# Optimization experiments

Hardware: AMD Instinct MI355X
Metric: run time of the kernel (lower is better)

Reference implementation:

```python
import jax, jax.numpy as jnp
import numpy as np


def setup_inputs() -> dict:
    key = jax.random.key(0)
    ks = jax.random.split(key, 5)
    b, t, e, h = 8, 1024, 256, 8
    w = lambda k, shape: jax.random.normal(k, shape, dtype=jnp.float32) * 0.02
    return {
        "x": jax.random.normal(ks[0], (b, t, e), dtype=jnp.float32),
        "Wq": w(ks[1], (e, e * h)), "bq": jnp.zeros((e * h,), jnp.float32),
        "Wk": w(ks[2], (e, e * h)), "bk": jnp.zeros((e * h,), jnp.float32),
        "Wv": w(ks[3], (e, e * h)), "bv": jnp.zeros((e * h,), jnp.float32),
        "Wu": w(ks[4], (e * h, e)), "bu": jnp.zeros((e,), jnp.float32),
    }


def reference(x, Wq, bq, Wk, bk, Wv, bv, Wu, bu):
    b, t, e = x.shape
    h = Wq.shape[1] // e  # each head has FULL width e in this module
    q = (x @ Wq + bq).reshape(b, t, h, e)
    k = (x @ Wk + bk).reshape(b, t, h, e)
    v = (x @ Wv + bv).reshape(b, t, h, e)
    # scores: (b, h, t, t), scaled by sqrt(e) as in the original
    scores = jnp.einsum('bihe,bjhe->bhij', q, k) / jnp.sqrt(jnp.asarray(e, jnp.float32))
    i = jnp.arange(t)[:, None]
    j = jnp.arange(t)[None, :]
    # mask mode 'first': triu(offset=0) -> -inf, i.e. query i sees only j < i
    scores = jnp.where(j >= i, -jnp.inf, scores)
    # row 0 is fully masked (torch softmax -> NaN, then zeroed post-softmax);
    # make it finite first so softmax is well-defined, then zero the attention row
    scores = jnp.where(i == 0, 0.0, scores)
    att = jax.nn.softmax(scores, axis=-1)
    att = jnp.where(i == 0, 0.0, att)
    out = jnp.einsum('bhij,bjhe->bihe', att, v).reshape(b, t, h * e)
    return out @ Wu + bu
```

## Files before the change

### kernel.cpp

```cpp
#include <hip/hip_runtime.h>

typedef unsigned short u16;
typedef short bf16x8 __attribute__((ext_vector_type(8)));
typedef float f32x4 __attribute__((ext_vector_type(4)));

static __device__ __forceinline__ u16 f2bf(float f) {
  union { float f; unsigned u; } a; a.f = f;
  unsigned r = a.u + 0x7fffu + ((a.u >> 16) & 1u);
  return (u16)(r >> 16);
}

static __device__ __forceinline__ bf16x8 as_bf(int4 v) {
  union { int4 i; bf16x8 b; } u; u.i = v; return u.b;
}

#define GLDS16(g, l)                                         \
  __builtin_amdgcn_global_load_lds(                          \
      (const __attribute__((address_space(1))) void*)(g),    \
      (__attribute__((address_space(3))) void*)(l), 16, 0, 0)

__global__ __launch_bounds__(256) void cvt_f32_bf16(const float* __restrict__ in,
                                                    u16* __restrict__ out, int n8) {
  int i = blockIdx.x * 256 + threadIdx.x;
  if (i >= n8) return;
  const float4* p = (const float4*)in + (size_t)i * 2;
  float4 a = p[0], b = p[1];
  union { u16 s[8]; int4 v; } u2;
  u2.s[0] = f2bf(a.x); u2.s[1] = f2bf(a.y); u2.s[2] = f2bf(a.z); u2.s[3] = f2bf(a.w);
  u2.s[4] = f2bf(b.x); u2.s[5] = f2bf(b.y); u2.s[6] = f2bf(b.z); u2.s[7] = f2bf(b.w);
  ((int4*)out)[i] = u2.v;
}

__global__ __launch_bounds__(256) void transpose_w(const float* __restrict__ in,
                                                   u16* __restrict__ out, int R, int C) {
  int T = blockIdx.x * 256 + threadIdx.x;
  int c = T % C;
  int rg = T / C;
  int r0 = rg * 32;
  __align__(16) u16 tmp[32];
#pragma unroll
  for (int j = 0; j < 32; ++j) tmp[j] = f2bf(in[(size_t)(r0 + j) * C + c]);
#pragma unroll
  for (int q = 0; q < 4; ++q)
    *(int4*)(out + (size_t)c * R + r0 + q * 8) = *(int4*)&tmp[q * 8];
}

__global__ __launch_bounds__(256) void transpose_v(const u16* __restrict__ V,
                                                   u16* __restrict__ Vt) {
  int T = blockIdx.x * 256 + threadIdx.x;
  int e = T & 255, tg = (T >> 8) & 31, bh = T >> 13;
  int b = bh >> 3, h = bh & 7;
  const u16* src = V + (size_t)(b * 1024 + tg * 32) * 2048 + h * 256 + e;
  __align__(16) u16 tmp[32];
#pragma unroll
  for (int j = 0; j < 32; ++j) tmp[j] = src[(size_t)j * 2048];
  u16* dst = Vt + (size_t)(bh * 256 + e) * 1024 + tg * 32;
#pragma unroll
  for (int q = 0; q < 4; ++q) *(int4*)(dst + q * 8) = *(int4*)&tmp[q * 8];
}

template <int BM, int BN, bool OUTBF>
__global__ __launch_bounds__(256) void gemm_bt(const u16* __restrict__ A,
                                               const u16* __restrict__ Bt,
                                               const float* __restrict__ bias0,
                                               const float* __restrict__ bias1,
                                               const float* __restrict__ bias2,
                                               void* __restrict__ Cout,
                                               int M, int N, int K) {
  constexpr int BK = 64;
  constexpr int TM = BM / 2 / 16, TN = BN / 2 / 16;
  constexpr int nA = BM / 32, nB = BN / 32;
  __shared__ int4 As4[BM * 8];
  __shared__ int4 Bs4[BN * 8];
  const int tid = threadIdx.x;
  const int w = tid >> 6, lane = tid & 63, lq = lane & 15, quad = lane >> 4;
  const int wm = w >> 1, wn = w & 1;
  const int m0 = blockIdx.y * BM, n0 = blockIdx.x * BN;
  const int z = blockIdx.z;

  const u16* Btz = Bt + (size_t)z * N * K;
  const float* bias = (z == 0) ? bias0 : (z == 1 ? bias1 : bias2);

  const int srow = lane >> 3;
  const int scb = (lane & 7) ^ ((lane >> 3) & 7);

  f32x4 acc[TM][TN];
#pragma unroll
  for (int mi = 0; mi < TM; ++mi)
#pragma unroll
    for (int ni = 0; ni < TN; ++ni) {
      f32x4 z4 = {0.f, 0.f, 0.f, 0.f};
      acc[mi][ni] = z4;
    }

  for (int k0 = 0; k0 < K; k0 += BK) {
    __syncthreads();
#pragma unroll
    for (int it = 0; it < nA; ++it) {
      int r = (w * nA + it) * 8 + srow;
      GLDS16(A + (size_t)(m0 + r) * K + k0 + scb * 8,
             (char*)As4 + (w * nA + it) * 1024);
    }
#pragma unroll
    for (int it = 0; it < nB; ++it) {
      int r = (w * nB + it) * 8 + srow;
      GLDS16(Btz + (size_t)(n0 + r) * K + k0 + scb * 8,
             (char*)Bs4 + (w * nB + it) * 1024);
    }
    __syncthreads();
#pragma unroll
    for (int kk = 0; kk < BK / 32; ++kk) {
      int4 af[TM], bf[TN];
#pragma unroll
      for (int mi = 0; mi < TM; ++mi) {
        int r = wm * (BM / 2) + mi * 16 + lq;
        af[mi] = As4[r * 8 + ((kk * 4 + quad) ^ (lq & 7))];
      }
#pragma unroll
      for (int ni = 0; ni < TN; ++ni) {
        int r = wn * (BN / 2) + ni * 16 + lq;
        bf[ni] = Bs4[r * 8 + ((kk * 4 + quad) ^ (lq & 7))];
      }
#pragma unroll
      for (int mi = 0; mi < TM; ++mi)
#pragma unroll
        for (int ni = 0; ni < TN; ++ni)
          acc[mi][ni] = __builtin_amdgcn_mfma_f32_16x16x32_bf16(
              as_bf(af[mi]), as_bf(bf[ni]), acc[mi][ni], 0, 0, 0);
    }
  }

#pragma unroll
  for (int mi = 0; mi < TM; ++mi)
#pragma unroll
    for (int ni = 0; ni < TN; ++ni)
#pragma unroll
      for (int r = 0; r < 4; ++r) {
        int row = m0 + wm * (BM / 2) + mi * 16 + quad * 4 + r;
        int col = n0 + wn * (BN / 2) + ni * 16 + lq;
        float v = acc[mi][ni][r] + bias[col];
        if constexpr (OUTBF)
          ((u16*)Cout)[(size_t)z * M * N + (size_t)row * N + col] = f2bf(v);
        else
          ((float*)Cout)[(size_t)row * N + col] = v;
      }
}

__global__ __launch_bounds__(256, 2) void attn_kernel(const u16* __restrict__ Q,
                                                      const u16* __restrict__ Km,
                                                      const u16* __restrict__ Vt,
                                                      u16* __restrict__ O) {
  const int bh = blockIdx.x;
  const int qt = 15 - blockIdx.y;
  const int b = bh >> 3, h = bh & 7;
  const int tid = threadIdx.x;
  const int w = tid >> 6, lane = tid & 63, lq = lane & 15, quad = lane >> 4;

  __shared__ int4 Ks4[2048];
  __shared__ int4 Vs4[2048];
  __shared__ u16 Ps[4096];
  u16* myPs = Ps + w * 1024;

  const int qg = qt * 64 + w * 16 + lq;
  const u16* qptr = Q + (size_t)(b * 1024 + qg) * 2048 + h * 256 + quad * 8;
  int4 qf[8];
#pragma unroll
  for (int kk = 0; kk < 8; ++kk) qf[kk] = *(const int4*)(qptr + kk * 32);

  int koffb[8], voffb[8];
  {
    const int kg = (lane & 31) >> 3;
#pragma unroll
    for (int it = 0; it < 8; ++it) {
      int r = w * 16 + it * 2 + (lane >> 5);
      int p = (lane & 7) ^ (r & 7);
      koffb[it] = r * 2048 + (kg * 8 + p) * 8;
      int rv = w * 64 + it * 8 + (lane >> 3);
      int cb = (lane & 7) ^ (rv & 7);
      voffb[it] = rv * 1024 + cb * 8;
    }
  }
  const u16* kbase = Km + (size_t)b * 1024 * 2048 + h * 256;
  const u16* vbase = Vt + (size_t)bh * 256 * 1024;

  f32x4 of[16];
#pragma unroll
  for (int i = 0; i < 16; ++i) {
    f32x4 z = {0.f, 0.f, 0.f, 0.f};
    of[i] = z;
  }
  float mst = -__builtin_inff(), lst = 0.f;

  for (int kt = 0; kt <= qt; ++kt) {
    __syncthreads();
    {
      const u16* kb = kbase + (size_t)kt * 64 * 2048;
      const u16* vb = vbase + kt * 64;
#pragma unroll
      for (int it = 0; it < 8; ++it)
        GLDS16(kb + koffb[it], (char*)Ks4 + (w * 8 + it) * 1024);
#pragma unroll
      for (int it = 0; it < 8; ++it)
        GLDS16(vb + voffb[it], (char*)Vs4 + (w * 8 + it) * 1024);
    }
    __syncthreads();

    f32x4 sc[4];
#pragma unroll
    for (int ns = 0; ns < 4; ++ns) {
      f32x4 a = {0.f, 0.f, 0.f, 0.f};
      int r = ns * 16 + lq;
#pragma unroll
      for (int kk = 0; kk < 8; ++kk) {
        int G = kk * 4 + quad;
        int4 kf = Ks4[r * 32 + (G >> 3) * 8 + ((G & 7) ^ (lq & 7))];
        a = __builtin_amdgcn_mfma_f32_16x16x32_bf16(as_bf(kf), as_bf(qf[kk]),
                                                    a, 0, 0, 0);
      }
      sc[ns] = a;
    }
#pragma unroll
    for (int ns = 0; ns < 4; ++ns) {
      int keyb = kt * 64 + ns * 16 + quad * 4;
#pragma unroll
      for (int r = 0; r < 4; ++r) {
        float v = sc[ns][r] * 0.0625f;
        sc[ns][r] = (keyb + r >= qg) ? -__builtin_inff() : v;
      }
    }
    float m16 = sc[0][0];
#pragma unroll
    for (int ns = 0; ns < 4; ++ns)
#pragma unroll
      for (int r = 0; r < 4; ++r) m16 = fmaxf(m16, sc[ns][r]);
    m16 = fmaxf(m16, __shfl_xor(m16, 16));
    m16 = fmaxf(m16, __shfl_xor(m16, 32));
    float mn = fmaxf(mst, m16);
    bool dead = (mn == -__builtin_inff());
    float alpha = dead ? 1.f : __expf(mst - mn);
    mst = mn;
    float s = 0.f;
#pragma unroll
    for (int ns = 0; ns < 4; ++ns)
#pragma unroll
      for (int r = 0; r < 4; ++r) {
        float p = dead ? 0.f : __expf(sc[ns][r] - mn);
        sc[ns][r] = p;
        s += p;
      }
    s += __shfl_xor(s, 16);
    s += __shfl_xor(s, 32);
    lst = lst * alpha + s;
#pragma unroll
    for (int i = 0; i < 16; ++i)
#pragma unroll
      for (int r = 0; r < 4; ++r) of[i][r] *= alpha;

#pragma unroll
    for (int ns = 0; ns < 4; ++ns) {
      int kb = ns * 2 + (quad >> 1);
      int base = lq * 64 + (kb ^ (lq & 7)) * 8 + (quad & 1) * 4;
#pragma unroll
      for (int h2 = 0; h2 < 2; ++h2) {
        unsigned d = (unsigned)f2bf(sc[ns][2 * h2]) |
                     ((unsigned)f2bf(sc[ns][2 * h2 + 1]) << 16);
        *(unsigned*)&myPs[base + 2 * h2] = d;
      }
    }
    int4 pf[2];
#pragma unroll
    for (int kk2 = 0; kk2 < 2; ++kk2) {
      int kbp = (kk2 * 4 + quad) ^ (lq & 7);
      pf[kk2] = *(const int4*)&myPs[lq * 64 + kbp * 8];
    }
#pragma unroll
    for (int ns2 = 0; ns2 < 16; ++ns2) {
      int r = ns2 * 16 + lq;
#pragma unroll
      for (int kk2 = 0; kk2 < 2; ++kk2) {
        int4 vf = Vs4[r * 8 + ((kk2 * 4 + quad) ^ (lq & 7))];
        of[ns2] = __builtin_amdgcn_mfma_f32_16x16x32_bf16(as_bf(vf), as_bf(pf[kk2]),
                                                          of[ns2], 0, 0, 0);
      }
    }
  }

  float inv = lst > 0.f ? 1.f / lst : 0.f;
  u16* optr = O + (size_t)(b * 1024 + qg) * 2048 + h * 256 + quad * 4;
#pragma unroll
  for (int ns2 = 0; ns2 < 16; ++ns2) {
    union { u16 s[4]; uint2 d; } o4;
#pragma unroll
    for (int r = 0; r < 4; ++r) o4.s[r] = f2bf(of[ns2][r] * inv);
    *(uint2*)(optr + ns2 * 16) = o4.d;
  }
}

#define WS_XB 0
#define WS_WQT 4194304
#define WS_WKT 5242880
#define WS_WVT 6291456
#define WS_WUT 7340032
#define WS_QW 8388608
#define WS_KW 41943040
#define WS_VW 75497472
#define WS_OW 75497472
#define WS_VTW 109051904

extern "C" void kernel_launch(void* const* d_in, const int* in_sizes, int n_in,
                              void* d_out, int out_size, void* d_ws, size_t ws_size,
                              hipStream_t stream) {
  const float* x = (const float*)d_in[0];
  const float* Wq = (const float*)d_in[1];
  const float* bq = (const float*)d_in[2];
  const float* Wk = (const float*)d_in[3];
  const float* bk = (const float*)d_in[4];
  const float* Wv = (const float*)d_in[5];
  const float* bv = (const float*)d_in[6];
  const float* Wu = (const float*)d_in[7];
  const float* bu = (const float*)d_in[8];
  float* out = (float*)d_out;

  char* ws = (char*)d_ws;
  u16* Xb = (u16*)(ws + WS_XB);
  u16* Wqt = (u16*)(ws + WS_WQT);
  u16* Wkt = (u16*)(ws + WS_WKT);
  u16* Wvt = (u16*)(ws + WS_WVT);
  u16* Wut = (u16*)(ws + WS_WUT);
  u16* Qw = (u16*)(ws + WS_QW);
  u16* Vw = (u16*)(ws + WS_VW);
  u16* Ow = (u16*)(ws + WS_OW);
  u16* Vtw = (u16*)(ws + WS_VTW);
  u16* Kw = (u16*)(ws + WS_KW);

  cvt_f32_bf16<<<1024, 256, 0, stream>>>(x, Xb, 262144);
  transpose_w<<<64, 256, 0, stream>>>(Wq, Wqt, 256, 2048);
  transpose_w<<<64, 256, 0, stream>>>(Wk, Wkt, 256, 2048);
  transpose_w<<<64, 256, 0, stream>>>(Wv, Wvt, 256, 2048);
  transpose_w<<<64, 256, 0, stream>>>(Wu, Wut, 2048, 256);

  gemm_bt<128, 128, true><<<dim3(16, 64, 3), 256, 0, stream>>>(
      Xb, Wqt, bq, bk, bv, Qw, 8192, 2048, 256);

  transpose_v<<<2048, 256, 0, stream>>>(Vw, Vtw);

  attn_kernel<<<dim3(64, 16), 256, 0, stream>>>(Qw, Kw, Vtw, Ow);

  gemm_bt<64, 64, false><<<dim3(4, 128, 1), 256, 0, stream>>>(
      Ow, Wut, bu, bu, bu, out, 8192, 256, 2048);
}
```

Baseline: 247.5 us.

## Fuse prep kernels, write V transposed from QKV GEMM, pair causal tiles in attention

The five conversion and weight-transpose launches are merged into one prep kernel. The QKV GEMM now writes V directly in transposed layout through an LDS staging step, which removes the separate transpose_v pass and one full round trip of V through memory. The attention kernel gives each block a short and a long causal query tile so work per block is even. It also switches to exp2 with the log2(e) factor folded into the scale and skips the output rescale when no lane's running max changes. The output GEMM tile becomes 128x64, and bf16 packing uses the hardware pair-convert intrinsic.

```diff
diff --git a/kernel.cpp b/kernel.cpp
--- a/kernel.cpp
+++ b/kernel.cpp
@@ -1,8 +1,11 @@
 #include <hip/hip_runtime.h>
+#include <hip/hip_bf16.h>
 
 typedef unsigned short u16;
 typedef short bf16x8 __attribute__((ext_vector_type(8)));
 typedef float f32x4 __attribute__((ext_vector_type(4)));
+
+#define EXP2(x) __builtin_amdgcn_exp2f(x)
 
 static __device__ __forceinline__ u16 f2bf(float f) {
   union { float f; unsigned u; } a; a.f = f;
@@ -10,6 +13,12 @@
   return (u16)(r >> 16);
 }
 
+static __device__ __forceinline__ unsigned pkbf(float a, float b) {
+  union { __hip_bfloat162 h; unsigned u; } c;
+  c.h = __float22bfloat162_rn(make_float2(a, b));
+  return c.u;
+}
+
 static __device__ __forceinline__ bf16x8 as_bf(int4 v) {
   union { int4 i; bf16x8 b; } u; u.i = v; return u.b;
 }
@@ -19,24 +28,32 @@
       (const __attribute__((address_space(1))) void*)(g),    \
       (__attribute__((address_space(3))) void*)(l), 16, 0, 0)
 
-__global__ __launch_bounds__(256) void cvt_f32_bf16(const float* __restrict__ in,
-                                                    u16* __restrict__ out, int n8) {
-  int i = blockIdx.x * 256 + threadIdx.x;
-  if (i >= n8) return;
-  const float4* p = (const float4*)in + (size_t)i * 2;
-  float4 a = p[0], b = p[1];
-  union { u16 s[8]; int4 v; } u2;
-  u2.s[0] = f2bf(a.x); u2.s[1] = f2bf(a.y); u2.s[2] = f2bf(a.z); u2.s[3] = f2bf(a.w);
-  u2.s[4] = f2bf(b.x); u2.s[5] = f2bf(b.y); u2.s[6] = f2bf(b.z); u2.s[7] = f2bf(b.w);
-  ((int4*)out)[i] = u2.v;
-}
-
-__global__ __launch_bounds__(256) void transpose_w(const float* __restrict__ in,
-                                                   u16* __restrict__ out, int R, int C) {
-  int T = blockIdx.x * 256 + threadIdx.x;
+__global__ __launch_bounds__(256) void prep(
+    const float* __restrict__ x, u16* __restrict__ Xb,
+    const float* __restrict__ Wq, u16* __restrict__ Wqt,
+    const float* __restrict__ Wk, u16* __restrict__ Wkt,
+    const float* __restrict__ Wv, u16* __restrict__ Wvt,
+    const float* __restrict__ Wu, u16* __restrict__ Wut) {
+  const int bid = blockIdx.x, tid = threadIdx.x;
+  if (bid < 1024) {
+    int i = bid * 256 + tid;
+    const float4* p = (const float4*)x + (size_t)i * 2;
+    float4 a = p[0], b = p[1];
+    union { unsigned s[4]; int4 v; } u2;
+    u2.s[0] = pkbf(a.x, a.y); u2.s[1] = pkbf(a.z, a.w);
+    u2.s[2] = pkbf(b.x, b.y); u2.s[3] = pkbf(b.z, b.w);
+    ((int4*)Xb)[i] = u2.v;
+    return;
+  }
+  const int which = (bid - 1024) >> 6;
+  const float* in; u16* out; int R, C;
+  if (which == 0)      { in = Wq; out = Wqt; R = 256;  C = 2048; }
+  else if (which == 1) { in = Wk; out = Wkt; R = 256;  C = 2048; }
+  else if (which == 2) { in = Wv; out = Wvt; R = 256;  C = 2048; }
+  else                 { in = Wu; out = Wut; R = 2048; C = 256;  }
+  int T = ((bid - 1024) & 63) * 256 + tid;
   int c = T % C;
-  int rg = T / C;
-  int r0 = rg * 32;
+  int r0 = (T / C) * 32;
   __align__(16) u16 tmp[32];
 #pragma unroll
   for (int j = 0; j < 32; ++j) tmp[j] = f2bf(in[(size_t)(r0 + j) * C + c]);
@@ -45,27 +62,122 @@
     *(int4*)(out + (size_t)c * R + r0 + q * 8) = *(int4*)&tmp[q * 8];
 }
 
-__global__ __launch_bounds__(256) void transpose_v(const u16* __restrict__ V,
-                                                   u16* __restrict__ Vt) {
-  int T = blockIdx.x * 256 + threadIdx.x;
-  int e = T & 255, tg = (T >> 8) & 31, bh = T >> 13;
-  int b = bh >> 3, h = bh & 7;
-  const u16* src = V + (size_t)(b * 1024 + tg * 32) * 2048 + h * 256 + e;
-  __align__(16) u16 tmp[32];
-#pragma unroll
-  for (int j = 0; j < 32; ++j) tmp[j] = src[(size_t)j * 2048];
-  u16* dst = Vt + (size_t)(bh * 256 + e) * 1024 + tg * 32;
-#pragma unroll
-  for (int q = 0; q < 4; ++q) *(int4*)(dst + q * 8) = *(int4*)&tmp[q * 8];
-}
-
-template <int BM, int BN, bool OUTBF>
+__global__ __launch_bounds__(256) void gemm_qkv(const u16* __restrict__ A,
+                                                const u16* __restrict__ Wt,
+                                                const float* __restrict__ bq,
+                                                const float* __restrict__ bk,
+                                                const float* __restrict__ bv,
+                                                u16* __restrict__ Qw,
+                                                u16* __restrict__ Kw,
+                                                u16* __restrict__ Vt) {
+  constexpr int BM = 128, BN = 128, BK = 64;
+  __shared__ int4 smem4[2048];
+  int4* As4 = smem4;
+  int4* Bs4 = smem4 + 1024;
+  const int tid = threadIdx.x;
+  const int w = tid >> 6, lane = tid & 63, lq = lane & 15, quad = lane >> 4;
+  const int wm = w >> 1, wn = w & 1;
+  const int m0 = blockIdx.y * BM, n0 = blockIdx.x * BN;
+  const int z = blockIdx.z;
+
+  const u16* Btz = Wt + (size_t)z * 2048 * 256;
+  const float* bias = (z == 0) ? bq : (z == 1 ? bk : bv);
+
+  const int srow = lane >> 3;
+  const int scb = (lane & 7) ^ ((lane >> 3) & 7);
+
+  f32x4 acc[4][4];
+#pragma unroll
+  for (int mi = 0; mi < 4; ++mi)
+#pragma unroll
+    for (int ni = 0; ni < 4; ++ni) {
+      f32x4 z4 = {0.f, 0.f, 0.f, 0.f};
+      acc[mi][ni] = z4;
+    }
+
+  for (int k0 = 0; k0 < 256; k0 += BK) {
+    __syncthreads();
+#pragma unroll
+    for (int it = 0; it < 4; ++it) {
+      int r = (w * 4 + it) * 8 + srow;
+      GLDS16(A + (size_t)(m0 + r) * 256 + k0 + scb * 8,
+             (char*)As4 + (w * 4 + it) * 1024);
+    }
+#pragma unroll
+    for (int it = 0; it < 4; ++it) {
+      int r = (w * 4 + it) * 8 + srow;
+      GLDS16(Btz + (size_t)(n0 + r) * 256 + k0 + scb * 8,
+             (char*)Bs4 + (w * 4 + it) * 1024);
+    }
+    __syncthreads();
+#pragma unroll
+    for (int kk = 0; kk < 2; ++kk) {
+      int4 af[4], bf[4];
+#pragma unroll
+      for (int mi = 0; mi < 4; ++mi) {
+        int r = wm * 64 + mi * 16 + lq;
+        af[mi] = As4[r * 8 + ((kk * 4 + quad) ^ (lq & 7))];
+      }
+#pragma unroll
+      for (int ni = 0; ni < 4; ++ni) {
+        int r = wn * 64 + ni * 16 + lq;
+        bf[ni] = Bs4[r * 8 + ((kk * 4 + quad) ^ (lq & 7))];
+      }
+#pragma unroll
+      for (int mi = 0; mi < 4; ++mi)
+#pragma unroll
+        for (int ni = 0; ni < 4; ++ni)
+          acc[mi][ni] = __builtin_amdgcn_mfma_f32_16x16x32_bf16(
+              as_bf(af[mi]), as_bf(bf[ni]), acc[mi][ni], 0, 0, 0);
+    }
+  }
+
+  if (z < 2) {
+    u16* Cout = z ? Kw : Qw;
+#pragma unroll
+    for (int mi = 0; mi < 4; ++mi)
+#pragma unroll
+      for (int ni = 0; ni < 4; ++ni)
+#pragma unroll
+        for (int r = 0; r < 4; ++r) {
+          int row = m0 + wm * 64 + mi * 16 + quad * 4 + r;
+          int col = n0 + wn * 64 + ni * 16 + lq;
+          Cout[(size_t)row * 2048 + col] = f2bf(acc[mi][ni][r] + bias[col]);
+        }
+  } else {
+    __syncthreads();
+    u16* Ts = (u16*)smem4;
+#pragma unroll
+    for (int mi = 0; mi < 4; ++mi)
+#pragma unroll
+      for (int ni = 0; ni < 4; ++ni) {
+        int c = wn * 64 + ni * 16 + lq;
+        int r0 = wm * 64 + mi * 16 + quad * 4;
+        float vb = bias[n0 + c];
+        uint2 dd;
+        dd.x = pkbf(acc[mi][ni][0] + vb, acc[mi][ni][1] + vb);
+        dd.y = pkbf(acc[mi][ni][2] + vb, acc[mi][ni][3] + vb);
+        *(uint2*)&Ts[c * 128 + (((r0 >> 3) ^ (c & 15)) << 3) + (r0 & 7)] = dd;
+      }
+    __syncthreads();
+    const int b = m0 >> 10, t0 = m0 & 1023;
+    const int e0 = n0 & 255, h = n0 >> 8;
+    const int bh = b * 8 + h;
+    const int i4 = tid & 15;
+#pragma unroll
+    for (int cc = 0; cc < 8; ++cc) {
+      int c = (tid >> 4) + cc * 16;
+      int4 val = *(const int4*)&Ts[c * 128 + ((i4 ^ (c & 15)) << 3)];
+      *(int4*)(Vt + (size_t)(bh * 256 + e0 + c) * 1024 + t0 + i4 * 8) = val;
+    }
+  }
+}
+
+template <int BM, int BN>
 __global__ __launch_bounds__(256) void gemm_bt(const u16* __restrict__ A,
                                                const u16* __restrict__ Bt,
-                                               const float* __restrict__ bias0,
-                                               const float* __restrict__ bias1,
-                                               const float* __restrict__ bias2,
-                                               void* __restrict__ Cout,
+                                               const float* __restrict__ bias,
+                                               float* __restrict__ Cout,
                                                int M, int N, int K) {
   constexpr int BK = 64;
   constexpr int TM = BM / 2 / 16, TN = BN / 2 / 16;
@@ -76,10 +188,6 @@
   const int w = tid >> 6, lane = tid & 63, lq = lane & 15, quad = lane >> 4;
   const int wm = w >> 1, wn = w & 1;
   const int m0 = blockIdx.y * BM, n0 = blockIdx.x * BN;
-  const int z = blockIdx.z;
-
-  const u16* Btz = Bt + (size_t)z * N * K;
-  const float* bias = (z == 0) ? bias0 : (z == 1 ? bias1 : bias2);
 
   const int srow = lane >> 3;
   const int scb = (lane & 7) ^ ((lane >> 3) & 7);
@@ -104,7 +212,7 @@
 #pragma unroll
     for (int it = 0; it < nB; ++it) {
       int r = (w * nB + it) * 8 + srow;
-      GLDS16(Btz + (size_t)(n0 + r) * K + k0 + scb * 8,
+      GLDS16(Bt + (size_t)(n0 + r) * K + k0 + scb * 8,
              (char*)Bs4 + (w * nB + it) * 1024);
     }
     __syncthreads();
@@ -138,11 +246,7 @@
       for (int r = 0; r < 4; ++r) {
         int row = m0 + wm * (BM / 2) + mi * 16 + quad * 4 + r;
         int col = n0 + wn * (BN / 2) + ni * 16 + lq;
-        float v = acc[mi][ni][r] + bias[col];
-        if constexpr (OUTBF)
-          ((u16*)Cout)[(size_t)z * M * N + (size_t)row * N + col] = f2bf(v);
-        else
-          ((float*)Cout)[(size_t)row * N + col] = v;
+        Cout[(size_t)row * N + col] = acc[mi][ni][r] + bias[col];
       }
 }
 
@@ -151,7 +255,7 @@
                                                       const u16* __restrict__ Vt,
                                                       u16* __restrict__ O) {
   const int bh = blockIdx.x;
-  const int qt = 15 - blockIdx.y;
+  const int pair = blockIdx.y;
   const int b = bh >> 3, h = bh & 7;
   const int tid = threadIdx.x;
   const int w = tid >> 6, lane = tid & 63, lq = lane & 15, quad = lane >> 4;
@@ -160,12 +264,6 @@
   __shared__ int4 Vs4[2048];
   __shared__ u16 Ps[4096];
   u16* myPs = Ps + w * 1024;
-
-  const int qg = qt * 64 + w * 16 + lq;
-  const u16* qptr = Q + (size_t)(b * 1024 + qg) * 2048 + h * 256 + quad * 8;
-  int4 qf[8];
-#pragma unroll
-  for (int kk = 0; kk < 8; ++kk) qf[kk] = *(const int4*)(qptr + kk * 32);
 
   int koffb[8], voffb[8];
   {
@@ -180,130 +278,139 @@
       voffb[it] = rv * 1024 + cb * 8;
     }
   }
-  const u16* kbase = Km + (size_t)b * 1024 * 2048 + h * 256;
-  const u16* vbase = Vt + (size_t)bh * 256 * 1024;
-
-  f32x4 of[16];
-#pragma unroll
-  for (int i = 0; i < 16; ++i) {
-    f32x4 z = {0.f, 0.f, 0.f, 0.f};
-    of[i] = z;
-  }
-  float mst = -__builtin_inff(), lst = 0.f;
-
-  for (int kt = 0; kt <= qt; ++kt) {
-    __syncthreads();
-    {
-      const u16* kb = kbase + (size_t)kt * 64 * 2048;
-      const u16* vb = vbase + kt * 64;
-#pragma unroll
-      for (int it = 0; it < 8; ++it)
-        GLDS16(kb + koffb[it], (char*)Ks4 + (w * 8 + it) * 1024);
-#pragma unroll
-      for (int it = 0; it < 8; ++it)
-        GLDS16(vb + voffb[it], (char*)Vs4 + (w * 8 + it) * 1024);
-    }
-    __syncthreads();
-
-    f32x4 sc[4];
-#pragma unroll
-    for (int ns = 0; ns < 4; ++ns) {
-      f32x4 a = {0.f, 0.f, 0.f, 0.f};
-      int r = ns * 16 + lq;
-#pragma unroll
-      for (int kk = 0; kk < 8; ++kk) {
-        int G = kk * 4 + quad;
-        int4 kf = Ks4[r * 32 + (G >> 3) * 8 + ((G & 7) ^ (lq & 7))];
-        a = __builtin_amdgcn_mfma_f32_16x16x32_bf16(as_bf(kf), as_bf(qf[kk]),
-                                                    a, 0, 0, 0);
-      }
-      sc[ns] = a;
-    }
-#pragma unroll
-    for (int ns = 0; ns < 4; ++ns) {
-      int keyb = kt * 64 + ns * 16 + quad * 4;
-#pragma unroll
-      for (int r = 0; r < 4; ++r) {
-        float v = sc[ns][r] * 0.0625f;
-        sc[ns][r] = (keyb + r >= qg) ? -__builtin_inff() : v;
-      }
-    }
-    float m16 = sc[0][0];
-#pragma unroll
-    for (int ns = 0; ns < 4; ++ns)
-#pragma unroll
-      for (int r = 0; r < 4; ++r) m16 = fmaxf(m16, sc[ns][r]);
-    m16 = fmaxf(m16, __shfl_xor(m16, 16));
-    m16 = fmaxf(m16, __shfl_xor(m16, 32));
-    float mn = fmaxf(mst, m16);
-    bool dead = (mn == -__builtin_inff());
-    float alpha = dead ? 1.f : __expf(mst - mn);
-    mst = mn;
-    float s = 0.f;
-#pragma unroll
-    for (int ns = 0; ns < 4; ++ns)
-#pragma unroll
-      for (int r = 0; r < 4; ++r) {
-        float p = dead ? 0.f : __expf(sc[ns][r] - mn);
-        sc[ns][r] = p;
-        s += p;
-      }
-    s += __shfl_xor(s, 16);
-    s += __shfl_xor(s, 32);
-    lst = lst * alpha + s;
-#pragma unroll
-    for (int i = 0; i < 16; ++i)
-#pragma unroll
-      for (int r = 0; r < 4; ++r) of[i][r] *= alpha;
-
-#pragma unroll
-    for (int ns = 0; ns < 4; ++ns) {
-      int kb = ns * 2 + (quad >> 1);
-      int base = lq * 64 + (kb ^ (lq & 7)) * 8 + (quad & 1) * 4;
-#pragma unroll
-      for (int h2 = 0; h2 < 2; ++h2) {
-        unsigned d = (unsigned)f2bf(sc[ns][2 * h2]) |
-                     ((unsigned)f2bf(sc[ns][2 * h2 + 1]) << 16);
-        *(unsigned*)&myPs[base + 2 * h2] = d;
-      }
-    }
-    int4 pf[2];
-#pragma unroll
-    for (int kk2 = 0; kk2 < 2; ++kk2) {
-      int kbp = (kk2 * 4 + quad) ^ (lq & 7);
-      pf[kk2] = *(const int4*)&myPs[lq * 64 + kbp * 8];
-    }
+  const u16* kbase = Km + (size_t)b * 2097152 + h * 256;
+  const u16* vbase = Vt + (size_t)bh * 262144;
+
+  const float SCL = 0.09016844f;
+  const float NEG = -3.0e38f;
+
+#pragma unroll 1
+  for (int hv = 0; hv < 2; ++hv) {
+    const int qt = hv ? (15 - pair) : pair;
+    const int qg = qt * 64 + w * 16 + lq;
+    const u16* qptr = Q + (size_t)(b * 1024 + qg) * 2048 + h * 256 + quad * 8;
+    int4 qf[8];
+#pragma unroll
+    for (int kk = 0; kk < 8; ++kk) qf[kk] = *(const int4*)(qptr + kk * 32);
+
+    f32x4 of[16];
+#pragma unroll
+    for (int i = 0; i < 16; ++i) {
+      f32x4 z = {0.f, 0.f, 0.f, 0.f};
+      of[i] = z;
+    }
+    float mst = NEG, lst = 0.f;
+
+    for (int kt = 0; kt <= qt; ++kt) {
+      __syncthreads();
+      {
+        const u16* kb = kbase + (size_t)kt * 131072;
+        const u16* vb = vbase + kt * 64;
+#pragma unroll
+        for (int it = 0; it < 8; ++it)
+          GLDS16(kb + koffb[it], (char*)Ks4 + (w * 8 + it) * 1024);
+#pragma unroll
+        for (int it = 0; it < 8; ++it)
+          GLDS16(vb + voffb[it], (char*)Vs4 + (w * 8 + it) * 1024);
+      }
+      __syncthreads();
+
+      f32x4 sc[4];
+#pragma unroll
+      for (int ns = 0; ns < 4; ++ns) {
+        f32x4 a = {0.f, 0.f, 0.f, 0.f};
+        int r = ns * 16 + lq;
+#pragma unroll
+        for (int kk = 0; kk < 8; ++kk) {
+          int G = kk * 4 + quad;
+          int4 kf = Ks4[r * 32 + (G >> 3) * 8 + ((G & 7) ^ (lq & 7))];
+          a = __builtin_amdgcn_mfma_f32_16x16x32_bf16(as_bf(kf), as_bf(qf[kk]),
+                                                      a, 0, 0, 0);
+        }
+        sc[ns] = a;
+      }
+#pragma unroll
+      for (int ns = 0; ns < 4; ++ns) {
+        int keyb = kt * 64 + ns * 16 + quad * 4;
+#pragma unroll
+        for (int r = 0; r < 4; ++r) {
+          float v = sc[ns][r] * SCL;
+          sc[ns][r] = (keyb + r >= qg) ? NEG : v;
+        }
+      }
+      float m16 = sc[0][0];
+#pragma unroll
+      for (int ns = 0; ns < 4; ++ns)
+#pragma unroll
+        for (int r = 0; r < 4; ++r) m16 = fmaxf(m16, sc[ns][r]);
+      m16 = fmaxf(m16, __shfl_xor(m16, 16));
+      m16 = fmaxf(m16, __shfl_xor(m16, 32));
+      if (__any(m16 > mst)) {
+        float mn = fmaxf(mst, m16);
+        float alpha = EXP2(mst - mn);
+        mst = mn;
+        lst *= alpha;
+#pragma unroll
+        for (int i = 0; i < 16; ++i)
+#pragma unroll
+          for (int r = 0; r < 4; ++r) of[i][r] *= alpha;
+      }
+      float s = 0.f;
+#pragma unroll
+      for (int ns = 0; ns < 4; ++ns)
+#pragma unroll
+        for (int r = 0; r < 4; ++r) {
+          float p = EXP2(sc[ns][r] - mst);
+          sc[ns][r] = p;
+          s += p;
+        }
+      s += __shfl_xor(s, 16);
+      s += __shfl_xor(s, 32);
+      lst += s;
+
+#pragma unroll
+      for (int ns = 0; ns < 4; ++ns) {
+        int kb2 = ns * 2 + (quad >> 1);
+        int base = lq * 64 + ((kb2 ^ (lq & 7)) << 3) + (quad & 1) * 4;
+        *(unsigned*)&myPs[base] = pkbf(sc[ns][0], sc[ns][1]);
+        *(unsigned*)&myPs[base + 2] = pkbf(sc[ns][2], sc[ns][3]);
+      }
+      int4 pf[2];
+#pragma unroll
+      for (int kk2 = 0; kk2 < 2; ++kk2) {
+        int kbp = (kk2 * 4 + quad) ^ (lq & 7);
+        pf[kk2] = *(const int4*)&myPs[lq * 64 + kbp * 8];
+      }
+#pragma unroll
+      for (int ns2 = 0; ns2 < 16; ++ns2) {
+        int r = ns2 * 16 + lq;
+#pragma unroll
+        for (int kk2 = 0; kk2 < 2; ++kk2) {
+          int4 vf = Vs4[r * 8 + ((kk2 * 4 + quad) ^ (lq & 7))];
+          of[ns2] = __builtin_amdgcn_mfma_f32_16x16x32_bf16(
+              as_bf(vf), as_bf(pf[kk2]), of[ns2], 0, 0, 0);
+        }
+      }
+    }
+
+    float inv = lst > 0.f ? 1.f / lst : 0.f;
+    if (qg == 0) inv = 0.f;
+    u16* optr = O + (size_t)(b * 1024 + qg) * 2048 + h * 256 + quad * 4;
 #pragma unroll
     for (int ns2 = 0; ns2 < 16; ++ns2) {
-      int r = ns2 * 16 + lq;
-#pragma unroll
-      for (int kk2 = 0; kk2 < 2; ++kk2) {
-        int4 vf = Vs4[r * 8 + ((kk2 * 4 + quad) ^ (lq & 7))];
-        of[ns2] = __builtin_amdgcn_mfma_f32_16x16x32_bf16(as_bf(vf), as_bf(pf[kk2]),
-                                                          of[ns2], 0, 0, 0);
-      }
-    }
-  }
-
-  float inv = lst > 0.f ? 1.f / lst : 0.f;
-  u16* optr = O + (size_t)(b * 1024 + qg) * 2048 + h * 256 + quad * 4;
-#pragma unroll
-  for (int ns2 = 0; ns2 < 16; ++ns2) {
-    union { u16 s[4]; uint2 d; } o4;
-#pragma unroll
-    for (int r = 0; r < 4; ++r) o4.s[r] = f2bf(of[ns2][r] * inv);
-    *(uint2*)(optr + ns2 * 16) = o4.d;
+      uint2 o4;
+      o4.x = pkbf(of[ns2][0] * inv, of[ns2][1] * inv);
+      o4.y = pkbf(of[ns2][2] * inv, of[ns2][3] * inv);
+      *(uint2*)(optr + ns2 * 16) = o4;
+    }
   }
 }
 
 #define WS_XB 0
 #define WS_WQT 4194304
-#define WS_WKT 5242880
-#define WS_WVT 6291456
 #define WS_WUT 7340032
 #define WS_QW 8388608
 #define WS_KW 41943040
-#define WS_VW 75497472
 #define WS_OW 75497472
 #define WS_VTW 109051904
 
@@ -324,28 +431,19 @@
   char* ws = (char*)d_ws;
   u16* Xb = (u16*)(ws + WS_XB);
   u16* Wqt = (u16*)(ws + WS_WQT);
-  u16* Wkt = (u16*)(ws + WS_WKT);
-  u16* Wvt = (u16*)(ws + WS_WVT);
+  u16* Wkt = Wqt + 524288;
+  u16* Wvt = Wqt + 1048576;
   u16* Wut = (u16*)(ws + WS_WUT);
   u16* Qw = (u16*)(ws + WS_QW);
-  u16* Vw = (u16*)(ws + WS_VW);
+  u16* Kw = (u16*)(ws + WS_KW);
   u16* Ow = (u16*)(ws + WS_OW);
   u16* Vtw = (u16*)(ws + WS_VTW);
-  u16* Kw = (u16*)(ws + WS_KW);
-
-  cvt_f32_bf16<<<1024, 256, 0, stream>>>(x, Xb, 262144);
-  transpose_w<<<64, 256, 0, stream>>>(Wq, Wqt, 256, 2048);
-  transpose_w<<<64, 256, 0, stream>>>(Wk, Wkt, 256, 2048);
-  transpose_w<<<64, 256, 0, stream>>>(Wv, Wvt, 256, 2048);
-  transpose_w<<<64, 256, 0, stream>>>(Wu, Wut, 2048, 256);
-
-  gemm_bt<128, 128, true><<<dim3(16, 64, 3), 256, 0, stream>>>(
-      Xb, Wqt, bq, bk, bv, Qw, 8192, 2048, 256);
-
-  transpose_v<<<2048, 256, 0, stream>>>(Vw, Vtw);
-
-  attn_kernel<<<dim3(64, 16), 256, 0, stream>>>(Qw, Kw, Vtw, Ow);
-
-  gemm_bt<64, 64, false><<<dim3(4, 128, 1), 256, 0, stream>>>(
-      Ow, Wut, bu, bu, bu, out, 8192, 256, 2048);
-}
+
+  prep<<<1280, 256, 0, stream>>>(x, Xb, Wq, Wqt, Wk, Wkt, Wv, Wvt, Wu, Wut);
+
+  gemm_qkv<<<dim3(16, 64, 3), 256, 0, stream>>>(Xb, Wqt, bq, bk, bv, Qw, Kw, Vtw);
+
+  attn_kernel<<<dim3(64, 8), 256, 0, stream>>>(Qw, Kw, Vtw, Ow);
+
+  gemm_bt<128, 64><<<dim3(4, 64), 256, 0, stream>>>(Ow, Wut, bu, out, 8192, 256, 2048);
+}
```

New measurement: 221.6 us. 10.5% less time.
